# Kernel optimization log

Hardware: AMD Instinct MI355X
Metric: run time of the kernel (lower is better)

The kernel has to match this reference:

```python
import jax, jax.numpy as jnp
import numpy as np

SEQ_LEN = 2048
EMBED_DIM = 1024
NUM_HEADS = 16
DIM_HEAD = EMBED_DIM // NUM_HEADS
BATCH = 4


def setup_inputs() -> dict:
    key = jax.random.key(0)
    k1, k2, k3 = jax.random.split(key, 3)
    x = jax.random.normal(k1, (SEQ_LEN, BATCH, EMBED_DIM), dtype=jnp.float32)
    weight_qkv = jax.random.normal(k2, (3 * EMBED_DIM, EMBED_DIM), dtype=jnp.float32) * (EMBED_DIM ** -0.5)
    weight_out = jax.random.normal(k3, (EMBED_DIM, EMBED_DIM), dtype=jnp.float32) * (EMBED_DIM ** -0.5)
    # causal mask: True where attention is DISALLOWED (strict upper triangle)
    mask = ~jnp.tril(jnp.ones((SEQ_LEN, SEQ_LEN), dtype=bool))[None, None]  # [1,1,L,L]
    return {"x": x, "weight_qkv": weight_qkv, "weight_out": weight_out, "mask": mask}


def reference(x, weight_qkv, weight_out, mask):
    L, N, E = x.shape
    H, Dh = NUM_HEADS, DIM_HEAD
    scale = Dh ** -0.5
    qkv = x @ weight_qkv.T                       # [L, N, 3E]
    q, k, v = jnp.split(qkv, 3, axis=-1)         # each [L, N, E]
    # [L, N, E] -> [N*H, L, Dh]
    def to_heads(t):
        return t.reshape(L, N * H, Dh).transpose(1, 0, 2)
    q, k, v = to_heads(q) * scale, to_heads(k), to_heads(v)
    attn = jnp.einsum('bld,bmd->blm', q, k)      # [N*H, L, L]
    attn = attn.reshape(N, H, L, L)
    attn = jnp.where(mask, jnp.float32(-100000.0), attn)
    attn = jax.nn.softmax(attn.reshape(N * H, L, L), axis=-1)
    out = jnp.einsum('blm,bmd->bld', attn, v)    # [N*H, L, Dh]
    out = out.transpose(1, 0, 2).reshape(L, N, E)
    return out @ weight_out.T
```

## Files before the change

kernel.cpp:

```cpp
#include <hip/hip_runtime.h>
#include <hip/hip_bf16.h>
#include <stdint.h>

constexpr int L  = 2048;
constexpr int NB = 4;
constexpr int E  = 1024;
constexpr int H  = 16;
constexpr int M  = L * NB;
constexpr int K  = E;
constexpr int QKV_LD = 3 * E;

typedef float  f32x4  __attribute__((ext_vector_type(4)));
typedef __bf16 bf16x4 __attribute__((ext_vector_type(4)));
typedef __bf16 bf16x8 __attribute__((ext_vector_type(8)));

#define AS1 __attribute__((address_space(1)))
#define AS3 __attribute__((address_space(3)))

static __device__ __forceinline__ void gl_lds16(const void* g, void* l) {
  __builtin_amdgcn_global_load_lds((const AS1 uint32_t*)g, (AS3 uint32_t*)l, 16, 0, 0);
}

__global__ __launch_bounds__(256)
void cvt_f32_bf16(const float* __restrict__ in, __bf16* __restrict__ out, int n4) {
  const int i = blockIdx.x * blockDim.x + threadIdx.x;
  if (i < n4) {
    const f32x4 v = ((const f32x4*)in)[i];
    bf16x4 o;
#pragma unroll
    for (int j = 0; j < 4; j++) o[j] = (__bf16)v[j];
    ((bf16x4*)out)[i] = o;
  }
}

template<int NC, typename OutT>
__global__ __launch_bounds__(256)
void gemm_bt(const __bf16* __restrict__ A, const __bf16* __restrict__ B,
             OutT* __restrict__ C) {
  constexpr int BK = 64;
  __shared__ char lds[2 * 128 * BK * 2];
  char* aL = lds;
  char* bL = lds + 128 * BK * 2;

  const int t    = threadIdx.x;
  const int lane = t & 63;
  const int w    = t >> 6;
  const int g    = lane >> 4;
  const int c    = lane & 15;

  const int rowBase = blockIdx.y * 128;
  const int colBase = blockIdx.x * 128;

  const int srow = t >> 3;
  const int scb  = (t & 7) * 16;
  const int ssw  = scb ^ ((srow & 7) << 4);

  const char* aSrcBase = (const char*)(A + (size_t)(rowBase + srow) * K) + ssw;
  const char* bSrcBase = (const char*)(B + (size_t)(colBase + srow) * K) + ssw;

  f32x4 acc[4][4];
#pragma unroll
  for (int i = 0; i < 4; i++)
#pragma unroll
    for (int j = 0; j < 4; j++) acc[i][j] = f32x4{0.f, 0.f, 0.f, 0.f};

  const int wr = (w >> 1) * 64;
  const int wc = (w & 1) * 64;

  for (int k0 = 0; k0 < K; k0 += BK) {
    __syncthreads();
#pragma unroll
    for (int q = 0; q < 4; q++) {
      gl_lds16(aSrcBase + (size_t)2 * k0 + (size_t)q * 32 * K * 2, aL + q * 4096 + t * 16);
      gl_lds16(bSrcBase + (size_t)2 * k0 + (size_t)q * 32 * K * 2, bL + q * 4096 + t * 16);
    }
    __syncthreads();

    bf16x8 af[4][2], bfR[4][2];
#pragma unroll
    for (int mi = 0; mi < 4; mi++) {
      const int row = wr + mi * 16 + c;
      const int sw  = (row & 7) << 4;
#pragma unroll
      for (int ks = 0; ks < 2; ks++)
        af[mi][ks] = *(const bf16x8*)(aL + row * 128 + ((ks * 64 + g * 16) ^ sw));
    }
#pragma unroll
    for (int ni = 0; ni < 4; ni++) {
      const int row = wc + ni * 16 + c;
      const int sw  = (row & 7) << 4;
#pragma unroll
      for (int ks = 0; ks < 2; ks++)
        bfR[ni][ks] = *(const bf16x8*)(bL + row * 128 + ((ks * 64 + g * 16) ^ sw));
    }
#pragma unroll
    for (int mi = 0; mi < 4; mi++)
#pragma unroll
      for (int ni = 0; ni < 4; ni++)
#pragma unroll
        for (int ks = 0; ks < 2; ks++)
          acc[mi][ni] = __builtin_amdgcn_mfma_f32_16x16x32_bf16(
              af[mi][ks], bfR[ni][ks], acc[mi][ni], 0, 0, 0);
  }

#pragma unroll
  for (int mi = 0; mi < 4; mi++)
#pragma unroll
    for (int ni = 0; ni < 4; ni++)
#pragma unroll
      for (int r = 0; r < 4; r++) {
        const int row = rowBase + wr + mi * 16 + g * 4 + r;
        const int col = colBase + wc + ni * 16 + c;
        C[(size_t)row * NC + col] = (OutT)acc[mi][ni][r];
      }
}

__global__ __launch_bounds__(256)
void transpose_v(const __bf16* __restrict__ qkv, __bf16* __restrict__ vT) {
  __shared__ char tile[64 * 160];
  const int lt = blockIdx.x;
  const int bh = blockIdx.y;
  const int n  = bh >> 4, h = bh & 15;
  const int t  = threadIdx.x;
  const int r8 = t >> 3;
  const int c8 = (t & 7) * 8;

#pragma unroll
  for (int q2 = 0; q2 < 2; q2++) {
    const int l = q2 * 32 + r8;
    const bf16x8 v = *(const bf16x8*)(qkv + (size_t)((lt * 64 + l) * 4 + n) * QKV_LD +
                                      2 * E + h * 64 + c8);
    *(bf16x8*)(tile + l * 160 + ((c8 * 2) ^ (((l >> 3) & 7) << 4))) = v;
  }
  __syncthreads();
#pragma unroll
  for (int q2 = 0; q2 < 2; q2++) {
    const int d = q2 * 32 + r8;
    bf16x8 o;
#pragma unroll
    for (int i = 0; i < 8; i++) {
      const int l = c8 + i;
      o[i] = *(const __bf16*)(tile + l * 160 + ((d * 2) ^ (((l >> 3) & 7) << 4)));
    }
    *(bf16x8*)(vT + ((size_t)bh * 64 + d) * 2048 + lt * 64 + c8) = o;
  }
}

__global__ __launch_bounds__(256)
void attn_kernel(const __bf16* __restrict__ qkv, const __bf16* __restrict__ vT,
                 __bf16* __restrict__ out) {
  const int qx = blockIdx.x;
  const int b  = blockIdx.y;
  const int n  = b >> 4;
  const int h  = b & 15;

  __shared__ char kl[64 * 128];
  __shared__ char vl[64 * 128];
  __shared__ char pl[4][16 * 128];

  const int t    = threadIdx.x;
  const int lane = t & 63;
  const int w    = t >> 6;
  const int g    = lane >> 4;
  const int c    = lane & 15;

  const int srow = t >> 3;
  const int scb  = (t & 7) * 16;
  const int kssw = scb ^ ((srow & 7) << 4);

  constexpr float QSCALE = 0.125f * 1.4426950408889634f;

  char* pw = pl[w];
  const int qloc = w * 16 + c;

  for (int pass = 0; pass < 2; ++pass) {
    const int qt = pass ? 31 - qx : qx;

    bf16x8 qa0, qa1;
    {
      const int qrow = qt * 64 + qloc;
      const __bf16* qp = qkv + (size_t)(qrow * 4 + n) * QKV_LD + h * 64;
      qa0 = *(const bf16x8*)(qp + g * 8);
      qa1 = *(const bf16x8*)(qp + 32 + g * 8);
#pragma unroll
      for (int i = 0; i < 8; i++) {
        qa0[i] = (__bf16)((float)qa0[i] * QSCALE);
        qa1[i] = (__bf16)((float)qa1[i] * QSCALE);
      }
    }

    float m_c = -3e38f, l_c = 0.f;
    f32x4 o[4];
#pragma unroll
    for (int ni = 0; ni < 4; ni++) o[ni] = f32x4{0.f, 0.f, 0.f, 0.f};

    for (int kt = 0; kt <= qt; ++kt) {
      __syncthreads();
#pragma unroll
      for (int q2 = 0; q2 < 2; q2++) {
        const int kvrow = kt * 64 + q2 * 32 + srow;
        gl_lds16((const char*)(qkv + (size_t)(kvrow * 4 + n) * QKV_LD + E + h * 64) + kssw,
                 kl + q2 * 4096 + t * 16);
        const int vd = q2 * 32 + srow;
        gl_lds16((const char*)(vT + ((size_t)b * 64 + vd) * 2048 + kt * 64) + kssw,
                 vl + q2 * 4096 + t * 16);
      }
      __syncthreads();

      f32x4 s[4];
#pragma unroll
      for (int ni = 0; ni < 4; ni++) s[ni] = f32x4{0.f, 0.f, 0.f, 0.f};
      __builtin_amdgcn_s_setprio(1);
#pragma unroll
      for (int ni = 0; ni < 4; ni++) {
        const int row = ni * 16 + c;
        const int sw  = (row & 7) << 4;
        const bf16x8 kb0 = *(const bf16x8*)(kl + row * 128 + ((g * 16) ^ sw));
        const bf16x8 kb1 = *(const bf16x8*)(kl + row * 128 + ((64 + g * 16) ^ sw));
        s[ni] = __builtin_amdgcn_mfma_f32_16x16x32_bf16(kb0, qa0, s[ni], 0, 0, 0);
        s[ni] = __builtin_amdgcn_mfma_f32_16x16x32_bf16(kb1, qa1, s[ni], 0, 0, 0);
      }
      __builtin_amdgcn_s_setprio(0);

      const bool lastTile = (kt == qt);
      float rmax = -3e38f;
#pragma unroll
      for (int ni = 0; ni < 4; ni++)
#pragma unroll
        for (int r = 0; r < 4; r++) {
          float v = s[ni][r];
          if (lastTile && (ni * 16 + g * 4 + r > qloc)) v = -3e38f;
          s[ni][r] = v;
          rmax = fmaxf(rmax, v);
        }
      rmax = fmaxf(rmax, __shfl_xor(rmax, 16));
      rmax = fmaxf(rmax, __shfl_xor(rmax, 32));

      const float mnew  = fmaxf(m_c, rmax);
      const float alpha = exp2f(m_c - mnew);
      const bool  grow  = rmax > m_c;
      m_c = mnew;

      float rsum = 0.f;
#pragma unroll
      for (int ni = 0; ni < 4; ni++)
#pragma unroll
        for (int r = 0; r < 4; r++) {
          const float e = exp2f(s[ni][r] - mnew);
          s[ni][r] = e;
          rsum += e;
        }
      rsum += __shfl_xor(rsum, 16);
      rsum += __shfl_xor(rsum, 32);
      l_c = l_c * alpha + rsum;

      if (__any(grow)) {
#pragma unroll
        for (int r = 0; r < 4; r++) {
          const float ar = __shfl(alpha, g * 4 + r);
#pragma unroll
          for (int ni = 0; ni < 4; ni++) o[ni][r] *= ar;
        }
      }

#pragma unroll
      for (int ni = 0; ni < 4; ni++) {
        bf16x4 pk;
#pragma unroll
        for (int r = 0; r < 4; r++) pk[r] = (__bf16)s[ni][r];
        *(bf16x4*)(pw + c * 128 + ((ni * 32 + g * 8) ^ ((c & 7) << 4))) = pk;
      }
      bf16x8 pa[2];
      {
        const int sw = (c & 7) << 4;
        pa[0] = *(const bf16x8*)(pw + c * 128 + ((g * 16) ^ sw));
        pa[1] = *(const bf16x8*)(pw + c * 128 + ((64 + g * 16) ^ sw));
      }
      __builtin_amdgcn_s_setprio(1);
#pragma unroll
      for (int ni = 0; ni < 4; ni++) {
        const int row = ni * 16 + c;
        const int sw  = (row & 7) << 4;
        const bf16x8 vb0 = *(const bf16x8*)(vl + row * 128 + ((g * 16) ^ sw));
        const bf16x8 vb1 = *(const bf16x8*)(vl + row * 128 + ((64 + g * 16) ^ sw));
        o[ni] = __builtin_amdgcn_mfma_f32_16x16x32_bf16(pa[0], vb0, o[ni], 0, 0, 0);
        o[ni] = __builtin_amdgcn_mfma_f32_16x16x32_bf16(pa[1], vb1, o[ni], 0, 0, 0);
      }
      __builtin_amdgcn_s_setprio(0);
    }

#pragma unroll
    for (int r = 0; r < 4; r++) {
      const float lr   = __shfl(l_c, g * 4 + r);
      const float inv  = 1.f / lr;
      const int   qrow = qt * 64 + w * 16 + g * 4 + r;
#pragma unroll
      for (int ni = 0; ni < 4; ni++) {
        const size_t off = (size_t)(qrow * 4 + n) * E + h * 64 + ni * 16 + c;
        out[off] = (__bf16)(o[ni][r] * inv);
      }
    }
  }
}

extern "C" void kernel_launch(void* const* d_in, const int* in_sizes, int n_in,
                              void* d_out, int out_size, void* d_ws, size_t ws_size,
                              hipStream_t stream) {
  const float* x    = (const float*)d_in[0];
  const float* wqkv = (const float*)d_in[1];
  const float* wout = (const float*)d_in[2];

  char* ws = (char*)d_ws;
  __bf16* x_bf    = (__bf16*)ws;                         ws += (size_t)M * E * 2;
  __bf16* wqkv_bf = (__bf16*)ws;                         ws += (size_t)QKV_LD * E * 2;
  __bf16* wout_bf = (__bf16*)ws;                         ws += (size_t)E * E * 2;
  __bf16* qkv     = (__bf16*)ws;                         ws += (size_t)M * QKV_LD * 2;
  __bf16* attno   = (__bf16*)ws;
  __bf16* vT      = x_bf;
  float*  outp    = (float*)d_out;

  cvt_f32_bf16<<<(M * E / 4) / 256, 256, 0, stream>>>(x, x_bf, M * E / 4);
  cvt_f32_bf16<<<(QKV_LD * E / 4) / 256, 256, 0, stream>>>(wqkv, wqkv_bf, QKV_LD * E / 4);
  cvt_f32_bf16<<<(E * E / 4) / 256, 256, 0, stream>>>(wout, wout_bf, E * E / 4);

  gemm_bt<QKV_LD, __bf16><<<dim3(QKV_LD / 128, M / 128), 256, 0, stream>>>(x_bf, wqkv_bf, qkv);
  transpose_v<<<dim3(L / 64, NB * H), 256, 0, stream>>>(qkv, vT);
  attn_kernel<<<dim3(16, NB * H), 256, 0, stream>>>(qkv, vT, attno);
  gemm_bt<E, float><<<dim3(E / 128, M / 128), 256, 0, stream>>>(attno, wout_bf, outp);
}
```

Measured before the change: 204.4 us.

## Process paired causal query tiles concurrently in 512-thread blocks with shared K/V loads

The attention kernel now uses 8 waves per block. Waves 0-3 handle query tile qx and waves 4-7 handle tile 31-qx at the same time, so both tiles share each K/V tile load instead of making two sequential passes. Each K/V tile is staged once per iteration with 512 threads. Waves whose diagonal is already reached sit idle but still take part in the block barriers. Softmax rescaling is now lazy and only runs when the row max grows by more than 8 in log2 units. This cuts exp and rescale work but lets unnormalised values grow larger before they are scaled back.

After: 234.2 us. 14.6% more time.

```diff
diff --git a/kernel.cpp b/kernel.cpp
--- a/kernel.cpp
+++ b/kernel.cpp
@@ -146,7 +146,7 @@
   }
 }
 
-__global__ __launch_bounds__(256)
+__global__ __launch_bounds__(512, 8)
 void attn_kernel(const __bf16* __restrict__ qkv, const __bf16* __restrict__ vT,
                  __bf16* __restrict__ out) {
   const int qx = blockIdx.x;
@@ -156,7 +156,7 @@
 
   __shared__ char kl[64 * 128];
   __shared__ char vl[64 * 128];
-  __shared__ char pl[4][16 * 128];
+  __shared__ char pl[8][16 * 128];
 
   const int t    = threadIdx.x;
   const int lane = t & 63;
@@ -171,134 +171,131 @@
   constexpr float QSCALE = 0.125f * 1.4426950408889634f;
 
   char* pw = pl[w];
-  const int qloc = w * 16 + c;
-
-  for (int pass = 0; pass < 2; ++pass) {
-    const int qt = pass ? 31 - qx : qx;
-
-    bf16x8 qa0, qa1;
+  const int qloc = (w & 3) * 16 + c;
+  const int qt   = (w < 4) ? qx : 31 - qx;
+  const int ktEnd = 31 - qx;
+
+  bf16x8 qa0, qa1;
+  {
+    const int qrow = qt * 64 + qloc;
+    const __bf16* qp = qkv + (size_t)(qrow * 4 + n) * QKV_LD + h * 64;
+    qa0 = *(const bf16x8*)(qp + g * 8);
+    qa1 = *(const bf16x8*)(qp + 32 + g * 8);
+#pragma unroll
+    for (int i = 0; i < 8; i++) {
+      qa0[i] = (__bf16)((float)qa0[i] * QSCALE);
+      qa1[i] = (__bf16)((float)qa1[i] * QSCALE);
+    }
+  }
+
+  float m_c = -3e38f, l_c = 0.f;
+  f32x4 o[4];
+#pragma unroll
+  for (int ni = 0; ni < 4; ni++) o[ni] = f32x4{0.f, 0.f, 0.f, 0.f};
+
+  for (int kt = 0; kt <= ktEnd; ++kt) {
+    __syncthreads();
     {
-      const int qrow = qt * 64 + qloc;
-      const __bf16* qp = qkv + (size_t)(qrow * 4 + n) * QKV_LD + h * 64;
-      qa0 = *(const bf16x8*)(qp + g * 8);
-      qa1 = *(const bf16x8*)(qp + 32 + g * 8);
-#pragma unroll
-      for (int i = 0; i < 8; i++) {
-        qa0[i] = (__bf16)((float)qa0[i] * QSCALE);
-        qa1[i] = (__bf16)((float)qa1[i] * QSCALE);
+      const int kvrow = kt * 64 + srow;
+      gl_lds16((const char*)(qkv + (size_t)(kvrow * 4 + n) * QKV_LD + E + h * 64) + kssw,
+               kl + t * 16);
+      gl_lds16((const char*)(vT + ((size_t)b * 64 + srow) * 2048 + kt * 64) + kssw,
+               vl + t * 16);
+    }
+    __syncthreads();
+
+    if (kt > qt) continue;
+
+    f32x4 s[4];
+#pragma unroll
+    for (int ni = 0; ni < 4; ni++) s[ni] = f32x4{0.f, 0.f, 0.f, 0.f};
+    __builtin_amdgcn_s_setprio(1);
+#pragma unroll
+    for (int ni = 0; ni < 4; ni++) {
+      const int row = ni * 16 + c;
+      const int sw  = (row & 7) << 4;
+      const bf16x8 kb0 = *(const bf16x8*)(kl + row * 128 + ((g * 16) ^ sw));
+      const bf16x8 kb1 = *(const bf16x8*)(kl + row * 128 + ((64 + g * 16) ^ sw));
+      s[ni] = __builtin_amdgcn_mfma_f32_16x16x32_bf16(kb0, qa0, s[ni], 0, 0, 0);
+      s[ni] = __builtin_amdgcn_mfma_f32_16x16x32_bf16(kb1, qa1, s[ni], 0, 0, 0);
+    }
+    __builtin_amdgcn_s_setprio(0);
+
+    const bool lastTile = (kt == qt);
+    float rmax = -3e38f;
+#pragma unroll
+    for (int ni = 0; ni < 4; ni++)
+#pragma unroll
+      for (int r = 0; r < 4; r++) {
+        float v = s[ni][r];
+        if (lastTile && (ni * 16 + g * 4 + r > qloc)) v = -3e38f;
+        s[ni][r] = v;
+        rmax = fmaxf(rmax, v);
       }
-    }
-
-    float m_c = -3e38f, l_c = 0.f;
-    f32x4 o[4];
-#pragma unroll
-    for (int ni = 0; ni < 4; ni++) o[ni] = f32x4{0.f, 0.f, 0.f, 0.f};
-
-    for (int kt = 0; kt <= qt; ++kt) {
-      __syncthreads();
-#pragma unroll
-      for (int q2 = 0; q2 < 2; q2++) {
-        const int kvrow = kt * 64 + q2 * 32 + srow;
-        gl_lds16((const char*)(qkv + (size_t)(kvrow * 4 + n) * QKV_LD + E + h * 64) + kssw,
-                 kl + q2 * 4096 + t * 16);
-        const int vd = q2 * 32 + srow;
-        gl_lds16((const char*)(vT + ((size_t)b * 64 + vd) * 2048 + kt * 64) + kssw,
-                 vl + q2 * 4096 + t * 16);
-      }
-      __syncthreads();
-
-      f32x4 s[4];
-#pragma unroll
-      for (int ni = 0; ni < 4; ni++) s[ni] = f32x4{0.f, 0.f, 0.f, 0.f};
-      __builtin_amdgcn_s_setprio(1);
-#pragma unroll
-      for (int ni = 0; ni < 4; ni++) {
-        const int row = ni * 16 + c;
-        const int sw  = (row & 7) << 4;
-        const bf16x8 kb0 = *(const bf16x8*)(kl + row * 128 + ((g * 16) ^ sw));
-        const bf16x8 kb1 = *(const bf16x8*)(kl + row * 128 + ((64 + g * 16) ^ sw));
-        s[ni] = __builtin_amdgcn_mfma_f32_16x16x32_bf16(kb0, qa0, s[ni], 0, 0, 0);
-        s[ni] = __builtin_amdgcn_mfma_f32_16x16x32_bf16(kb1, qa1, s[ni], 0, 0, 0);
-      }
-      __builtin_amdgcn_s_setprio(0);
-
-      const bool lastTile = (kt == qt);
-      float rmax = -3e38f;
-#pragma unroll
-      for (int ni = 0; ni < 4; ni++)
-#pragma unroll
-        for (int r = 0; r < 4; r++) {
-          float v = s[ni][r];
-          if (lastTile && (ni * 16 + g * 4 + r > qloc)) v = -3e38f;
-          s[ni][r] = v;
-          rmax = fmaxf(rmax, v);
-        }
-      rmax = fmaxf(rmax, __shfl_xor(rmax, 16));
-      rmax = fmaxf(rmax, __shfl_xor(rmax, 32));
-
+    rmax = fmaxf(rmax, __shfl_xor(rmax, 16));
+    rmax = fmaxf(rmax, __shfl_xor(rmax, 32));
+
+    if (__any(rmax > m_c + 8.f)) {
       const float mnew  = fmaxf(m_c, rmax);
       const float alpha = exp2f(m_c - mnew);
-      const bool  grow  = rmax > m_c;
+      l_c *= alpha;
+#pragma unroll
+      for (int r = 0; r < 4; r++) {
+        const float ar = __shfl(alpha, g * 4 + r);
+#pragma unroll
+        for (int ni = 0; ni < 4; ni++) o[ni][r] *= ar;
+      }
       m_c = mnew;
-
-      float rsum = 0.f;
-#pragma unroll
-      for (int ni = 0; ni < 4; ni++)
-#pragma unroll
-        for (int r = 0; r < 4; r++) {
-          const float e = exp2f(s[ni][r] - mnew);
-          s[ni][r] = e;
-          rsum += e;
-        }
-      rsum += __shfl_xor(rsum, 16);
-      rsum += __shfl_xor(rsum, 32);
-      l_c = l_c * alpha + rsum;
-
-      if (__any(grow)) {
-#pragma unroll
-        for (int r = 0; r < 4; r++) {
-          const float ar = __shfl(alpha, g * 4 + r);
-#pragma unroll
-          for (int ni = 0; ni < 4; ni++) o[ni][r] *= ar;
-        }
+    }
+
+    float rsum = 0.f;
+#pragma unroll
+    for (int ni = 0; ni < 4; ni++)
+#pragma unroll
+      for (int r = 0; r < 4; r++) {
+        const float e = exp2f(s[ni][r] - m_c);
+        s[ni][r] = e;
+        rsum += e;
       }
-
-#pragma unroll
-      for (int ni = 0; ni < 4; ni++) {
-        bf16x4 pk;
-#pragma unroll
-        for (int r = 0; r < 4; r++) pk[r] = (__bf16)s[ni][r];
-        *(bf16x4*)(pw + c * 128 + ((ni * 32 + g * 8) ^ ((c & 7) << 4))) = pk;
-      }
-      bf16x8 pa[2];
-      {
-        const int sw = (c & 7) << 4;
-        pa[0] = *(const bf16x8*)(pw + c * 128 + ((g * 16) ^ sw));
-        pa[1] = *(const bf16x8*)(pw + c * 128 + ((64 + g * 16) ^ sw));
-      }
-      __builtin_amdgcn_s_setprio(1);
-#pragma unroll
-      for (int ni = 0; ni < 4; ni++) {
-        const int row = ni * 16 + c;
-        const int sw  = (row & 7) << 4;
-        const bf16x8 vb0 = *(const bf16x8*)(vl + row * 128 + ((g * 16) ^ sw));
-        const bf16x8 vb1 = *(const bf16x8*)(vl + row * 128 + ((64 + g * 16) ^ sw));
-        o[ni] = __builtin_amdgcn_mfma_f32_16x16x32_bf16(pa[0], vb0, o[ni], 0, 0, 0);
-        o[ni] = __builtin_amdgcn_mfma_f32_16x16x32_bf16(pa[1], vb1, o[ni], 0, 0, 0);
-      }
-      __builtin_amdgcn_s_setprio(0);
-    }
-
-#pragma unroll
-    for (int r = 0; r < 4; r++) {
-      const float lr   = __shfl(l_c, g * 4 + r);
-      const float inv  = 1.f / lr;
-      const int   qrow = qt * 64 + w * 16 + g * 4 + r;
-#pragma unroll
-      for (int ni = 0; ni < 4; ni++) {
-        const size_t off = (size_t)(qrow * 4 + n) * E + h * 64 + ni * 16 + c;
-        out[off] = (__bf16)(o[ni][r] * inv);
-      }
+    rsum += __shfl_xor(rsum, 16);
+    rsum += __shfl_xor(rsum, 32);
+    l_c += rsum;
+
+#pragma unroll
+    for (int ni = 0; ni < 4; ni++) {
+      bf16x4 pk;
+#pragma unroll
+      for (int r = 0; r < 4; r++) pk[r] = (__bf16)s[ni][r];
+      *(bf16x4*)(pw + c * 128 + ((ni * 32 + g * 8) ^ ((c & 7) << 4))) = pk;
+    }
+    bf16x8 pa[2];
+    {
+      const int sw = (c & 7) << 4;
+      pa[0] = *(const bf16x8*)(pw + c * 128 + ((g * 16) ^ sw));
+      pa[1] = *(const bf16x8*)(pw + c * 128 + ((64 + g * 16) ^ sw));
+    }
+    __builtin_amdgcn_s_setprio(1);
+#pragma unroll
+    for (int ni = 0; ni < 4; ni++) {
+      const int row = ni * 16 + c;
+      const int sw  = (row & 7) << 4;
+      const bf16x8 vb0 = *(const bf16x8*)(vl + row * 128 + ((g * 16) ^ sw));
+      const bf16x8 vb1 = *(const bf16x8*)(vl + row * 128 + ((64 + g * 16) ^ sw));
+      o[ni] = __builtin_amdgcn_mfma_f32_16x16x32_bf16(pa[0], vb0, o[ni], 0, 0, 0);
+      o[ni] = __builtin_amdgcn_mfma_f32_16x16x32_bf16(pa[1], vb1, o[ni], 0, 0, 0);
+    }
+    __builtin_amdgcn_s_setprio(0);
+  }
+
+#pragma unroll
+  for (int r = 0; r < 4; r++) {
+    const float lr   = __shfl(l_c, g * 4 + r);
+    const float inv  = 1.f / lr;
+    const int   qrow = qt * 64 + (w & 3) * 16 + g * 4 + r;
+#pragma unroll
+    for (int ni = 0; ni < 4; ni++) {
+      const size_t off = (size_t)(qrow * 4 + n) * E + h * 64 + ni * 16 + c;
+      out[off] = (__bf16)(o[ni][r] * inv);
     }
   }
 }
@@ -325,6 +322,6 @@
 
   gemm_bt<QKV_LD, __bf16><<<dim3(QKV_LD / 128, M / 128), 256, 0, stream>>>(x_bf, wqkv_bf, qkv);
   transpose_v<<<dim3(L / 64, NB * H), 256, 0, stream>>>(qkv, vT);
-  attn_kernel<<<dim3(16, NB * H), 256, 0, stream>>>(qkv, vT, attno);
+  attn_kernel<<<dim3(16, NB * H), 512, 0, stream>>>(qkv, vT, attno);
   gemm_bt<E, float><<<dim3(E / 128, M / 128), 256, 0, stream>>>(attno, wout_bf, outp);
 }
```

## Double-buffer K/V tiles in LDS and lazily rescale the softmax accumulator

Applied to the files above, without the earlier changes.

Adds a second LDS buffer for the K and V tiles so the next tile's global-to-LDS loads are issued before computing on the current tile. This removes one barrier per iteration and is meant to hide global load latency behind the MFMA and softmax work. The online softmax now rescales the running max and the output accumulator only when the new row max exceeds the stored max by more than 8 in log2 space. That skips most rescale shuffles, in exchange for slightly larger unnormalized intermediate values. The change doubles K/V LDS usage and relies on the top-of-loop barrier also waiting for the asynchronous LDS loads to finish.

After: 204.4 us. No clear change (-0.0%).

```diff
diff --git a/kernel.cpp b/kernel.cpp
--- a/kernel.cpp
+++ b/kernel.cpp
@@ -154,8 +154,8 @@
   const int n  = b >> 4;
   const int h  = b & 15;
 
-  __shared__ char kl[64 * 128];
-  __shared__ char vl[64 * 128];
+  __shared__ char kl[2][64 * 128];
+  __shared__ char vl[2][64 * 128];
   __shared__ char pl[4][16 * 128];
 
   const int t    = threadIdx.x;
@@ -172,6 +172,8 @@
 
   char* pw = pl[w];
   const int qloc = w * 16 + c;
+
+  int cur = 0;
 
   for (int pass = 0; pass < 2; ++pass) {
     const int qt = pass ? 31 - qx : qx;
@@ -194,18 +196,34 @@
 #pragma unroll
     for (int ni = 0; ni < 4; ni++) o[ni] = f32x4{0.f, 0.f, 0.f, 0.f};
 
+#pragma unroll
+    for (int q2 = 0; q2 < 2; q2++) {
+      const int kvrow = q2 * 32 + srow;
+      gl_lds16((const char*)(qkv + (size_t)(kvrow * 4 + n) * QKV_LD + E + h * 64) + kssw,
+               kl[cur] + q2 * 4096 + t * 16);
+      gl_lds16((const char*)(vT + ((size_t)b * 64 + q2 * 32 + srow) * 2048) + kssw,
+               vl[cur] + q2 * 4096 + t * 16);
+    }
+
     for (int kt = 0; kt <= qt; ++kt) {
       __syncthreads();
-#pragma unroll
-      for (int q2 = 0; q2 < 2; q2++) {
-        const int kvrow = kt * 64 + q2 * 32 + srow;
-        gl_lds16((const char*)(qkv + (size_t)(kvrow * 4 + n) * QKV_LD + E + h * 64) + kssw,
-                 kl + q2 * 4096 + t * 16);
-        const int vd = q2 * 32 + srow;
-        gl_lds16((const char*)(vT + ((size_t)b * 64 + vd) * 2048 + kt * 64) + kssw,
-                 vl + q2 * 4096 + t * 16);
-      }
-      __syncthreads();
+
+      if (kt < qt) {
+        const int nx = kt + 1;
+#pragma unroll
+        for (int q2 = 0; q2 < 2; q2++) {
+          const int kvrow = nx * 64 + q2 * 32 + srow;
+          gl_lds16((const char*)(qkv + (size_t)(kvrow * 4 + n) * QKV_LD + E + h * 64) + kssw,
+                   kl[cur ^ 1] + q2 * 4096 + t * 16);
+          const int vd = q2 * 32 + srow;
+          gl_lds16((const char*)(vT + ((size_t)b * 64 + vd) * 2048 + nx * 64) + kssw,
+                   vl[cur ^ 1] + q2 * 4096 + t * 16);
+        }
+      }
+      __builtin_amdgcn_sched_barrier(0);
+
+      const char* klc = kl[cur];
+      const char* vlc = vl[cur];
 
       f32x4 s[4];
 #pragma unroll
@@ -215,8 +233,8 @@
       for (int ni = 0; ni < 4; ni++) {
         const int row = ni * 16 + c;
         const int sw  = (row & 7) << 4;
-        const bf16x8 kb0 = *(const bf16x8*)(kl + row * 128 + ((g * 16) ^ sw));
-        const bf16x8 kb1 = *(const bf16x8*)(kl + row * 128 + ((64 + g * 16) ^ sw));
+        const bf16x8 kb0 = *(const bf16x8*)(klc + row * 128 + ((g * 16) ^ sw));
+        const bf16x8 kb1 = *(const bf16x8*)(klc + row * 128 + ((64 + g * 16) ^ sw));
         s[ni] = __builtin_amdgcn_mfma_f32_16x16x32_bf16(kb0, qa0, s[ni], 0, 0, 0);
         s[ni] = __builtin_amdgcn_mfma_f32_16x16x32_bf16(kb1, qa1, s[ni], 0, 0, 0);
       }
@@ -236,32 +254,31 @@
       rmax = fmaxf(rmax, __shfl_xor(rmax, 16));
       rmax = fmaxf(rmax, __shfl_xor(rmax, 32));
 
-      const float mnew  = fmaxf(m_c, rmax);
-      const float alpha = exp2f(m_c - mnew);
-      const bool  grow  = rmax > m_c;
-      m_c = mnew;
+      if (__any(rmax > m_c + 8.f)) {
+        const float mnew  = fmaxf(m_c, rmax);
+        const float alpha = exp2f(m_c - mnew);
+        l_c *= alpha;
+#pragma unroll
+        for (int r = 0; r < 4; r++) {
+          const float ar = __shfl(alpha, g * 4 + r);
+#pragma unroll
+          for (int ni = 0; ni < 4; ni++) o[ni][r] *= ar;
+        }
+        m_c = mnew;
+      }
 
       float rsum = 0.f;
 #pragma unroll
       for (int ni = 0; ni < 4; ni++)
 #pragma unroll
         for (int r = 0; r < 4; r++) {
-          const float e = exp2f(s[ni][r] - mnew);
+          const float e = exp2f(s[ni][r] - m_c);
           s[ni][r] = e;
           rsum += e;
         }
       rsum += __shfl_xor(rsum, 16);
       rsum += __shfl_xor(rsum, 32);
-      l_c = l_c * alpha + rsum;
-
-      if (__any(grow)) {
-#pragma unroll
-        for (int r = 0; r < 4; r++) {
-          const float ar = __shfl(alpha, g * 4 + r);
-#pragma unroll
-          for (int ni = 0; ni < 4; ni++) o[ni][r] *= ar;
-        }
-      }
+      l_c += rsum;
 
 #pragma unroll
       for (int ni = 0; ni < 4; ni++) {
@@ -281,12 +298,14 @@
       for (int ni = 0; ni < 4; ni++) {
         const int row = ni * 16 + c;
         const int sw  = (row & 7) << 4;
-        const bf16x8 vb0 = *(const bf16x8*)(vl + row * 128 + ((g * 16) ^ sw));
-        const bf16x8 vb1 = *(const bf16x8*)(vl + row * 128 + ((64 + g * 16) ^ sw));
+        const bf16x8 vb0 = *(const bf16x8*)(vlc + row * 128 + ((g * 16) ^ sw));
+        const bf16x8 vb1 = *(const bf16x8*)(vlc + row * 128 + ((64 + g * 16) ^ sw));
         o[ni] = __builtin_amdgcn_mfma_f32_16x16x32_bf16(pa[0], vb0, o[ni], 0, 0, 0);
         o[ni] = __builtin_amdgcn_mfma_f32_16x16x32_bf16(pa[1], vb1, o[ni], 0, 0, 0);
       }
       __builtin_amdgcn_s_setprio(0);
+
+      cur ^= 1;
     }
 
 #pragma unroll
```
